# Optimization experiments

Measured on AMD Instinct MI355X. Metric: run time of the kernel, lower is better.

Reference implementation:

```python
import jax, jax.numpy as jnp
import numpy as np

B, S1, S2, S3, I, O = 4, 64, 64, 64, 32, 32
MX, MZ = 16, 16
HID = O * 2  # factor=2 feedforward hidden


def setup_inputs() -> dict:
    key = jax.random.key(0)
    ks = jax.random.split(key, 5)
    x = jax.random.normal(ks[0], (B, S1, S2, S3, I), jnp.float32)
    # xavier-normal-ish scale for complex fourier weights stored as [...,2]
    sw = np.float32(np.sqrt(2.0 / (I + O)))
    wx = jax.random.normal(ks[1], (I, O, MX, 2), jnp.float32) * sw
    wz = jax.random.normal(ks[2], (I, O, MZ, 2), jnp.float32) * sw
    w1 = jax.random.normal(ks[3], (O, HID), jnp.float32) * np.float32(np.sqrt(1.0 / O))
    b1 = jnp.zeros((HID,), jnp.float32)
    w2 = jax.random.normal(ks[4], (HID, O), jnp.float32) * np.float32(np.sqrt(1.0 / HID))
    b2 = jnp.zeros((O,), jnp.float32)
    return {"x": x, "wx": wx, "wz": wz, "w1": w1, "b1": b1, "w2": w2, "b2": b2}


def _forward_fourier(x, wx, wz):
    # x: [b, i, s1, s2, s3]
    # z-axis branch
    cwz = wz[..., 0] + 1j * wz[..., 1]          # [i, o, mz] complex
    xfz = jnp.fft.rfft(x, axis=-1, norm='ortho')  # [b,i,s1,s2,S3//2+1]
    pz = jnp.einsum('bixyz,ioz->boxyz', xfz[..., :MZ], cwz)
    pz = jnp.pad(pz, ((0, 0), (0, 0), (0, 0), (0, 0), (0, S3 // 2 + 1 - MZ)))
    xz = jnp.fft.irfft(pz, n=S3, axis=-1, norm='ortho')
    # x-axis branch (note: modes_y branch contributes 0 in the source, xy=0.0)
    cwx = wx[..., 0] + 1j * wx[..., 1]          # [i, o, mx]
    xfx = jnp.fft.rfft(x, axis=2, norm='ortho')  # [b,i,S1//2+1,s2,s3]
    px = jnp.einsum('bixyz,iox->boxyz', xfx[:, :, :MX], cwx)
    px = jnp.pad(px, ((0, 0), (0, 0), (0, S1 // 2 + 1 - MX), (0, 0), (0, 0)))
    xx = jnp.fft.irfft(px, n=S1, axis=2, norm='ortho')
    return xx + xz


def reference(x, wx, wz, w1, b1, w2, b2):
    xt = jnp.transpose(x, (0, 4, 1, 2, 3))      # b i s1 s2 s3
    y = _forward_fourier(xt, wx, wz)
    y = jnp.transpose(y, (0, 2, 3, 4, 1))       # b s1 s2 s3 o
    # backcast FeedForward: Linear -> ReLU -> Linear (dropout=0, no norms)
    h = jax.nn.relu(y @ w1 + b1)
    b_out = h @ w2 + b2
    return b_out
```

## Files before the change

### kernel.cpp

```cpp
#include <hip/hip_runtime.h>

namespace {

typedef _Float16 half_t;
typedef half_t f16x8 __attribute__((ext_vector_type(8)));
typedef float f32x4 __attribute__((ext_vector_type(4)));

constexpr size_t RSTR = 64 * 64 * 32;

constexpr int WS_TF = 0;
constexpr int WS_TI = 2048;
constexpr int WS_WZ = 4096;
constexpr int WS_WX = 69632;
constexpr int WS_W1 = 135168;
constexpr int WS_W2 = 137216;

__device__ __forceinline__ float f4get(const float4& v, int u) {
  return u == 0 ? v.x : (u == 1 ? v.y : (u == 2 ? v.z : v.w));
}

__device__ __forceinline__ f32x4 mfma16(f16x8 a, f16x8 b, f32x4 c) {
  return __builtin_amdgcn_mfma_f32_16x16x32_f16(a, b, c, 0, 0, 0);
}

__global__ __launch_bounds__(256) void kinit(const float* __restrict__ wx,
                                             const float* __restrict__ wz,
                                             const float* __restrict__ w1,
                                             const float* __restrict__ w2,
                                             half_t* __restrict__ wsh) {
  const int id = blockIdx.x * 256 + threadIdx.x;
  const int l = id & 63, r = l & 15, g = l >> 4;
  f16x8 frag;
  if (id < 256) {
    int fid = id >> 6, mt = fid >> 1, kt = fid & 1;
#pragma unroll
    for (int e = 0; e < 8; ++e) {
      int k = kt * 32 + 8 * g + e;
      int mc = mt * 16 + r, m = mc >> 1, p = mc & 1;
      float s, c;
      sincospif((float)(m * k) * (1.0f / 32.0f), &s, &c);
      frag[e] = (half_t)(0.125f * (p ? -s : c));
    }
    *(f16x8*)(wsh + WS_TF + (size_t)id * 8) = frag;
  } else if (id < 512) {
    int id2 = id - 256, mt = id2 >> 6;
#pragma unroll
    for (int e = 0; e < 8; ++e) {
      int zp = mt * 16 + r;
      int k = 8 * g + e, m = k >> 1, p = k & 1;
      float s, c;
      sincospif((float)(m * zp) * (1.0f / 32.0f), &s, &c);
      float sc = (m == 0) ? 0.125f : 0.25f;
      frag[e] = (half_t)(p ? -sc * s : sc * c);
    }
    *(f16x8*)(wsh + WS_TI + (size_t)id2 * 8) = frag;
  } else if (id < 16896) {
    int id2 = id - 512;
    const float* wsrc = wz;
    size_t off = WS_WZ;
    if (id2 >= 8192) { id2 -= 8192; wsrc = wx; off = WS_WX; }
    int fid = id2 >> 6, m = fid >> 3, kt = (fid >> 2) & 1, nt = fid & 3;
#pragma unroll
    for (int e = 0; e < 8; ++e) {
      int k = kt * 32 + 8 * g + e, i = k >> 1, p = k & 1;
      int n = nt * 16 + r, o = n >> 1, q = n & 1;
      int base = ((i * 32 + o) * 16 + m) * 2;
      float re = wsrc[base], im = wsrc[base + 1];
      frag[e] = (half_t)(q ? (p ? re : im) : (p ? -im : re));
    }
    *(f16x8*)(wsh + off + (size_t)id2 * 8) = frag;
  } else if (id < 17152) {
    int id2 = id - 16896, nt = id2 >> 6;
#pragma unroll
    for (int e = 0; e < 8; ++e) {
      int k = 8 * g + e, n = nt * 16 + r;
      frag[e] = (half_t)w1[k * 64 + n];
    }
    *(f16x8*)(wsh + WS_W1 + (size_t)id2 * 8) = frag;
  } else if (id < 17408) {
    int id2 = id - 17152, fid = id2 >> 6, kt = fid >> 1, nt = fid & 1;
#pragma unroll
    for (int e = 0; e < 8; ++e) {
      int k = kt * 32 + 8 * g + e, n = nt * 16 + r;
      frag[e] = (half_t)w2[k * 32 + n];
    }
    *(f16x8*)(wsh + WS_W2 + (size_t)id2 * 8) = frag;
  }
}

template <int BR>
__global__ __launch_bounds__(256) void kspec(const float* __restrict__ x,
                                             const half_t* __restrict__ wsh,
                                             const float* __restrict__ b1g,
                                             const float* __restrict__ b2g,
                                             float* __restrict__ outf) {
  __shared__ __align__(16) char smraw[49152];
  half_t* XB = (half_t*)smraw;
  half_t* FB = (half_t*)smraw;
  half_t* PB = (half_t*)(smraw + 32768);
  half_t* outh = (half_t*)outf;
  const int t = threadIdx.x, l = t & 63, w = t >> 6, r = l & 15, g = l >> 4;
  const f32x4 vzero = {0.f, 0.f, 0.f, 0.f};

  const int col0 = blockIdx.x * 8;
  size_t xbase = (size_t)col0 * 2048, zstr = 32, cstr = 2048;

  {
    int c = t >> 5, sub = t & 31;
    int i4 = (sub & 7) * 4, zq = sub >> 3;
    const float* xp = x + xbase + (size_t)c * cstr + i4;
#pragma unroll
    for (int zo = 0; zo < 2; ++zo) {
      int zb = zq * 16 + zo * 8;
      float4 v[8];
#pragma unroll
      for (int zz = 0; zz < 8; ++zz)
        v[zz] = *(const float4*)(xp + (size_t)(zb + zz) * zstr);
#pragma unroll
      for (int u = 0; u < 4; ++u) {
        f16x8 rowv;
#pragma unroll
        for (int zz = 0; zz < 8; ++zz) rowv[zz] = (half_t)f4get(v[zz], u);
        int rowi = c * 32 + i4 + u;
        int gr = (zb >> 3) ^ (rowi & 7);
        *(f16x8*)(XB + rowi * 64 + gr * 8) = rowv;
      }
    }
  }
  __syncthreads();

  f32x4 fa[2][4];
#pragma unroll
  for (int mt = 0; mt < 2; ++mt)
#pragma unroll
    for (int nt = 0; nt < 4; ++nt) fa[mt][nt] = vzero;
  {
    f16x8 Atf[2][2], Bx[4][2];
#pragma unroll
    for (int mt = 0; mt < 2; ++mt)
#pragma unroll
      for (int kt = 0; kt < 2; ++kt)
        Atf[mt][kt] = *(const f16x8*)(wsh + WS_TF + (size_t)((mt * 2 + kt) * 64 + l) * 8);
#pragma unroll
    for (int nt = 0; nt < 4; ++nt)
#pragma unroll
      for (int kt = 0; kt < 2; ++kt) {
        int rowi = w * 64 + nt * 16 + r;
        int gr = (kt * 4 + g) ^ (rowi & 7);
        Bx[nt][kt] = *(const f16x8*)(XB + rowi * 64 + gr * 8);
      }
#pragma unroll
    for (int kt = 0; kt < 2; ++kt)
#pragma unroll
      for (int nt = 0; nt < 4; ++nt)
#pragma unroll
        for (int mt = 0; mt < 2; ++mt)
          fa[mt][nt] = mfma16(Atf[mt][kt], Bx[nt][kt], fa[mt][nt]);
  }
  __syncthreads();

#pragma unroll
  for (int mt = 0; mt < 2; ++mt)
#pragma unroll
    for (int nt = 0; nt < 4; ++nt)
#pragma unroll
      for (int q = 0; q < 4; ++q) {
        int mc = mt * 16 + 4 * g + q, m = mc >> 1, p = mc & 1;
        int n = w * 64 + nt * 16 + r, c = n >> 5, i = n & 31;
        int k = 2 * i + p;
        FB[(m * 16 + c) * 64 + ((k >> 3) ^ (c & 7)) * 8 + (k & 7)] = (half_t)fa[mt][nt][q];
      }
  __syncthreads();

  const half_t* WF = wsh + WS_WZ;
#pragma unroll
  for (int j = 0; j < 4; ++j) {
    int m = w * 4 + j;
    f16x8 Af[2];
#pragma unroll
    for (int kt = 0; kt < 2; ++kt) {
      int gr = (kt * 4 + g) ^ (r & 7);
      Af[kt] = *(const f16x8*)(FB + (m * 16 + r) * 64 + gr * 8);
    }
    f32x4 pa[4];
#pragma unroll
    for (int nt = 0; nt < 4; ++nt) pa[nt] = vzero;
#pragma unroll
    for (int kt = 0; kt < 2; ++kt)
#pragma unroll
      for (int nt = 0; nt < 4; ++nt) {
        f16x8 Bw = *(const f16x8*)(WF + (size_t)((m * 8 + kt * 4 + nt) * 64 + l) * 8);
        pa[nt] = mfma16(Af[kt], Bw, pa[nt]);
      }
#pragma unroll
    for (int nt = 0; nt < 4; ++nt)
#pragma unroll
      for (int q = 0; q < 4; ++q) {
        int c = 4 * g + q;
        if (c < 8) {
          int n = nt * 16 + r, o = n >> 1, q2 = n & 1;
          int k = 2 * m + q2;
          PB[(c * 32 + o) * 32 + ((k >> 3) ^ (o & 3)) * 8 + (k & 7)] = (half_t)pa[nt][q];
        }
      }
  }
  __syncthreads();

  {
    f16x8 Ati[4];
#pragma unroll
    for (int mt = 0; mt < 4; ++mt)
      Ati[mt] = *(const f16x8*)(wsh + WS_TI + (size_t)(mt * 64 + l) * 8);
#pragma unroll
    for (int cc = 0; cc < 2; ++cc) {
      int c = w * 2 + cc;
      f16x8 Bp[2];
#pragma unroll
      for (int nt = 0; nt < 2; ++nt) {
        int o = nt * 16 + r;
        Bp[nt] = *(const f16x8*)(PB + (c * 32 + o) * 32 + (g ^ (o & 3)) * 8);
      }
      f32x4 ya[4][2];
#pragma unroll
      for (int mt = 0; mt < 4; ++mt)
#pragma unroll
        for (int nt = 0; nt < 2; ++nt) ya[mt][nt] = mfma16(Ati[mt], Bp[nt], vzero);
#pragma unroll
      for (int mt = 0; mt < 4; ++mt)
#pragma unroll
        for (int nt = 0; nt < 2; ++nt)
#pragma unroll
          for (int q = 0; q < 4; ++q) {
            int zp = mt * 16 + 4 * g + q, o = nt * 16 + r;
            outh[(size_t)(col0 + c) * 4096 + zp * 64 + o] = (half_t)ya[mt][nt][q];
          }
    }
  }
}

__global__ __launch_bounds__(256, 5) void kx4(const float* __restrict__ x,
                                              const half_t* __restrict__ wsh,
                                              const float* __restrict__ b1g,
                                              const float* __restrict__ b2g,
                                              float* __restrict__ outf) {
  __shared__ __align__(16) half_t smh[16384];
  half_t* XB = smh;
  half_t* FB = smh + 8192;
  half_t* PB = smh + 12288;
  half_t* YL = smh;
  half_t* HL = smh + 8192;
  half_t* outh = (half_t*)outf;
  const int t = threadIdx.x, l = t & 63, w = t >> 6, r = l & 15, g = l >> 4;
  const f32x4 vzero = {0.f, 0.f, 0.f, 0.f};

  const int d = blockIdx.x;
  const int p = (d & 7) * 512 + (d >> 3);
  const int col0 = p * 4;
  const int b = col0 >> 12, s2 = (col0 >> 6) & 63, s30 = col0 & 63;
  const size_t xbase = (size_t)b * 8388608 + (size_t)s2 * 2048 + (size_t)s30 * 32;

  {
    int sub = t & 31, zq = t >> 5;
    int c = sub >> 3, i4 = (sub & 7) * 4;
    const float* xp = x + xbase + (size_t)c * 32 + i4 + (size_t)(zq * 8) * RSTR;
    float4 v[8];
#pragma unroll
    for (int zz = 0; zz < 8; ++zz) v[zz] = *(const float4*)(xp + (size_t)zz * RSTR);
#pragma unroll
    for (int uu = 0; uu < 4; ++uu) {
      int u = (uu + sub) & 3;
      f16x8 rowv;
#pragma unroll
      for (int zz = 0; zz < 8; ++zz) rowv[zz] = (half_t)f4get(v[zz], u);
      int rowi = c * 32 + i4 + u;
      *(f16x8*)(XB + rowi * 64 + (zq ^ (rowi & 7)) * 8) = rowv;
    }
  }
  __syncthreads();

  f32x4 fa[2][2];
  {
    f16x8 Atf[2][2], Bx[2][2];
#pragma unroll
    for (int mt = 0; mt < 2; ++mt)
#pragma unroll
      for (int kt = 0; kt < 2; ++kt)
        Atf[mt][kt] = *(const f16x8*)(wsh + WS_TF + (size_t)((mt * 2 + kt) * 64 + l) * 8);
#pragma unroll
    for (int nt = 0; nt < 2; ++nt)
#pragma unroll
      for (int kt = 0; kt < 2; ++kt) {
        int rowi = w * 32 + nt * 16 + r;
        Bx[nt][kt] = *(const f16x8*)(XB + rowi * 64 + (((kt * 4 + g) ^ (rowi & 7))) * 8);
      }
#pragma unroll
    for (int mt = 0; mt < 2; ++mt)
#pragma unroll
      for (int nt = 0; nt < 2; ++nt) fa[mt][nt] = vzero;
#pragma unroll
    for (int kt = 0; kt < 2; ++kt)
#pragma unroll
      for (int nt = 0; nt < 2; ++nt)
#pragma unroll
        for (int mt = 0; mt < 2; ++mt)
          fa[mt][nt] = mfma16(Atf[mt][kt], Bx[nt][kt], fa[mt][nt]);
  }
#pragma unroll
  for (int mt = 0; mt < 2; ++mt)
#pragma unroll
    for (int nt = 0; nt < 2; ++nt)
#pragma unroll
      for (int q = 0; q < 4; ++q) {
        int mc = mt * 16 + 4 * g + q, m = mc >> 1, pp = mc & 1;
        int n = w * 32 + nt * 16 + r, c = n >> 5, i = n & 31;
        int k = 2 * i + pp;
        FB[(m * 4 + c) * 64 + (((k >> 3) ^ ((m + 2 * c) & 7))) * 8 + (k & 7)] =
            (half_t)fa[mt][nt][q];
      }
  __syncthreads();

#pragma unroll
  for (int j = 0; j < 4; ++j) {
    int m = w * 4 + j;
    int rsel = r & 3, keym = (m + 2 * rsel) & 7;
    f16x8 Af[2];
#pragma unroll
    for (int kt = 0; kt < 2; ++kt)
      Af[kt] = *(const f16x8*)(FB + (m * 4 + rsel) * 64 + (((kt * 4 + g) ^ keym)) * 8);
    f32x4 pa[4];
#pragma unroll
    for (int nt = 0; nt < 4; ++nt) pa[nt] = vzero;
#pragma unroll
    for (int kt = 0; kt < 2; ++kt)
#pragma unroll
      for (int nt = 0; nt < 4; ++nt) {
        f16x8 Bw = *(const f16x8*)(wsh + WS_WX + (size_t)((m * 8 + kt * 4 + nt) * 64 + l) * 8);
        pa[nt] = mfma16(Af[kt], Bw, pa[nt]);
      }
    if (g == 0) {
#pragma unroll
      for (int nt = 0; nt < 4; ++nt)
#pragma unroll
        for (int q = 0; q < 4; ++q) {
          int c = q;
          int n = nt * 16 + r, o = n >> 1, q2 = n & 1;
          int k = 2 * m + q2;
          PB[(c * 32 + o) * 32 + (((k >> 3) ^ (o & 3))) * 8 + (k & 7)] = (half_t)pa[nt][q];
        }
    }
  }
  __syncthreads();

  {
    half_t yzr[4][2][4];
    const half_t* yzp = outh + ((size_t)b * 4096 + s2) * 4096 + (size_t)(s30 + w) * 64 +
                        (size_t)(4 * g) * 262144 + r;
#pragma unroll
    for (int mt = 0; mt < 4; ++mt)
#pragma unroll
      for (int q = 0; q < 4; ++q)
#pragma unroll
        for (int nt = 0; nt < 2; ++nt)
          yzr[mt][nt][q] = yzp[(size_t)(mt * 16 + q) * 262144 + nt * 16];

    f16x8 Ati[4], Bp[2];
#pragma unroll
    for (int mt = 0; mt < 4; ++mt)
      Ati[mt] = *(const f16x8*)(wsh + WS_TI + (size_t)(mt * 64 + l) * 8);
#pragma unroll
    for (int nt = 0; nt < 2; ++nt) {
      int o = nt * 16 + r;
      Bp[nt] = *(const f16x8*)(PB + (w * 32 + o) * 32 + ((g ^ (o & 3))) * 8);
    }
    f32x4 ya[4][2];
#pragma unroll
    for (int mt = 0; mt < 4; ++mt)
#pragma unroll
      for (int nt = 0; nt < 2; ++nt) ya[mt][nt] = mfma16(Ati[mt], Bp[nt], vzero);
#pragma unroll
    for (int mt = 0; mt < 4; ++mt)
#pragma unroll
      for (int nt = 0; nt < 2; ++nt)
#pragma unroll
        for (int q = 0; q < 4; ++q) {
          int zp = mt * 16 + 4 * g + q, o = nt * 16 + r;
          float acc = ya[mt][nt][q] + (float)yzr[mt][nt][q];
          int rowi = w * 64 + zp;
          YL[rowi * 32 + (((o >> 3) ^ ((rowi >> 2) & 3))) * 8 + (o & 7)] = (half_t)acc;
        }
  }
  __syncthreads();

  {
    f16x8 W1F[4], W2F[4];
#pragma unroll
    for (int nt = 0; nt < 4; ++nt)
      W1F[nt] = *(const f16x8*)(wsh + WS_W1 + (size_t)(nt * 64 + l) * 8);
#pragma unroll
    for (int f = 0; f < 4; ++f)
      W2F[f] = *(const f16x8*)(wsh + WS_W2 + (size_t)(f * 64 + l) * 8);
    float b1v[4], b2v[2];
#pragma unroll
    for (int nt = 0; nt < 4; ++nt) b1v[nt] = b1g[nt * 16 + r];
#pragma unroll
    for (int nt = 0; nt < 2; ++nt) b2v[nt] = b2g[nt * 16 + r];

    for (int rr = 0; rr < 4; ++rr) {
      int rowA = rr * 64 + w * 16 + r;
      f16x8 AY = *(const f16x8*)(YL + rowA * 32 + ((g ^ ((rowA >> 2) & 3))) * 8);
      f32x4 ha[4];
#pragma unroll
      for (int nt = 0; nt < 4; ++nt) ha[nt] = mfma16(AY, W1F[nt], vzero);
#pragma unroll
      for (int nt = 0; nt < 4; ++nt)
#pragma unroll
        for (int q = 0; q < 4; ++q) {
          int rloc = w * 16 + 4 * g + q, n = nt * 16 + r;
          float hv = fmaxf(ha[nt][q] + b1v[nt], 0.f);
          HL[rloc * 64 + (((n >> 3) ^ ((rloc >> 2) & 7))) * 8 + (n & 7)] = (half_t)hv;
        }
      __syncthreads();
      int rowA2 = w * 16 + r;
      f16x8 AH[2];
#pragma unroll
      for (int kt = 0; kt < 2; ++kt)
        AH[kt] = *(const f16x8*)(HL + rowA2 * 64 + (((kt * 4 + g) ^ ((rowA2 >> 2) & 7))) * 8);
      f32x4 oa[2];
#pragma unroll
      for (int nt = 0; nt < 2; ++nt) oa[nt] = vzero;
#pragma unroll
      for (int kt = 0; kt < 2; ++kt)
#pragma unroll
        for (int nt = 0; nt < 2; ++nt) oa[nt] = mfma16(AH[kt], W2F[kt * 2 + nt], oa[nt]);
#pragma unroll
      for (int nt = 0; nt < 2; ++nt)
#pragma unroll
        for (int q = 0; q < 4; ++q) {
          int zp2 = w * 16 + 4 * g + q, o = nt * 16 + r;
          outf[(size_t)b * 8388608 + (size_t)zp2 * RSTR + (size_t)s2 * 2048 +
               (size_t)(s30 + rr) * 32 + o] = oa[nt][q] + b2v[nt];
        }
      if (rr < 3) __syncthreads();
    }
  }
}

}

extern "C" void kernel_launch(void* const* d_in, const int* in_sizes, int n_in,
                              void* d_out, int out_size, void* d_ws, size_t ws_size,
                              hipStream_t stream) {
  const float* x = (const float*)d_in[0];
  const float* wx = (const float*)d_in[1];
  const float* wz = (const float*)d_in[2];
  const float* w1 = (const float*)d_in[3];
  const float* b1 = (const float*)d_in[4];
  const float* w2 = (const float*)d_in[5];
  const float* b2 = (const float*)d_in[6];
  float* out = (float*)d_out;
  half_t* wsh = (half_t*)d_ws;

  hipLaunchKernelGGL(kinit, dim3(68), dim3(256), 0, stream, wx, wz, w1, w2, wsh);
  hipLaunchKernelGGL((kspec<0>), dim3(2048), dim3(256), 0, stream, x, wsh, b1, b2, out);
  hipLaunchKernelGGL(kx4, dim3(4096), dim3(256), 0, stream, x, wsh, b1, b2, out);
}
```

Measured before the change: 135.5 us.

## Hoist global loads early, pack FB stores, and halve FFN sync rounds

Issues the yz half-precision gather and the W1/W2/bias fragment loads at kernel start, before the LDS stages, so their latency overlaps the DFT and mode-mixing work. FB writes are packed as f16x2 pairs. The feed-forward loop now processes two 16-row tiles per wave per iteration, which cuts the number of block barriers from 7 to 3. Occupancy hint drops from 5 to 4 blocks per CU to make room for the extra live registers.

```diff
diff --git a/kernel.cpp b/kernel.cpp
--- a/kernel.cpp
+++ b/kernel.cpp
@@ -3,6 +3,7 @@
 namespace {
 
 typedef _Float16 half_t;
+typedef half_t f16x2 __attribute__((ext_vector_type(2)));
 typedef half_t f16x8 __attribute__((ext_vector_type(8)));
 typedef float f32x4 __attribute__((ext_vector_type(4)));
 
@@ -238,7 +239,7 @@
   }
 }
 
-__global__ __launch_bounds__(256, 5) void kx4(const float* __restrict__ x,
+__global__ __launch_bounds__(256, 4) void kx4(const float* __restrict__ x,
                                               const half_t* __restrict__ wsh,
                                               const float* __restrict__ b1g,
                                               const float* __restrict__ b2g,
@@ -259,20 +260,34 @@
   const int b = col0 >> 12, s2 = (col0 >> 6) & 63, s30 = col0 & 63;
   const size_t xbase = (size_t)b * 8388608 + (size_t)s2 * 2048 + (size_t)s30 * 32;
 
-  {
-    int sub = t & 31, zq = t >> 5;
-    int c = sub >> 3, i4 = (sub & 7) * 4;
-    const float* xp = x + xbase + (size_t)c * 32 + i4 + (size_t)(zq * 8) * RSTR;
-    float4 v[8];
-#pragma unroll
-    for (int zz = 0; zz < 8; ++zz) v[zz] = *(const float4*)(xp + (size_t)zz * RSTR);
+  const int sub = t & 31, zq = t >> 5;
+  const int sc = sub >> 3, si4 = (sub & 7) * 4;
+  const float* xp = x + xbase + (size_t)sc * 32 + si4 + (size_t)(zq * 8) * RSTR;
+  float4 v[8];
+#pragma unroll
+  for (int zz = 0; zz < 8; ++zz) v[zz] = *(const float4*)(xp + (size_t)zz * RSTR);
+
+  half_t yzr[4][2][4];
+  {
+    const half_t* yzp = outh + ((size_t)b * 4096 + s2) * 4096 + (size_t)(s30 + w) * 64 +
+                        (size_t)(4 * g) * 262144 + r;
+#pragma unroll
+    for (int mt = 0; mt < 4; ++mt)
+#pragma unroll
+      for (int q = 0; q < 4; ++q)
+#pragma unroll
+        for (int nt = 0; nt < 2; ++nt)
+          yzr[mt][nt][q] = yzp[(size_t)(mt * 16 + q) * 262144 + nt * 16];
+  }
+
+  {
 #pragma unroll
     for (int uu = 0; uu < 4; ++uu) {
       int u = (uu + sub) & 3;
       f16x8 rowv;
 #pragma unroll
       for (int zz = 0; zz < 8; ++zz) rowv[zz] = (half_t)f4get(v[zz], u);
-      int rowi = c * 32 + i4 + u;
+      int rowi = sc * 32 + si4 + u;
       *(f16x8*)(XB + rowi * 64 + (zq ^ (rowi & 7)) * 8) = rowv;
     }
   }
@@ -310,12 +325,14 @@
 #pragma unroll
     for (int nt = 0; nt < 2; ++nt)
 #pragma unroll
-      for (int q = 0; q < 4; ++q) {
-        int mc = mt * 16 + 4 * g + q, m = mc >> 1, pp = mc & 1;
+      for (int pr = 0; pr < 2; ++pr) {
+        int q = 2 * pr;
+        int mc = mt * 16 + 4 * g + q, m = mc >> 1;
         int n = w * 32 + nt * 16 + r, c = n >> 5, i = n & 31;
-        int k = 2 * i + pp;
-        FB[(m * 4 + c) * 64 + (((k >> 3) ^ ((m + 2 * c) & 7))) * 8 + (k & 7)] =
-            (half_t)fa[mt][nt][q];
+        int k = 2 * i;
+        f16x2 pairv = {(half_t)fa[mt][nt][q], (half_t)fa[mt][nt][q + 1]};
+        *(f16x2*)(FB + (m * 4 + c) * 64 + (((k >> 3) ^ ((m + 2 * c) & 7))) * 8 + (k & 7)) =
+            pairv;
       }
   __syncthreads();
 
@@ -349,20 +366,22 @@
         }
     }
   }
-  __syncthreads();
-
-  {
-    half_t yzr[4][2][4];
-    const half_t* yzp = outh + ((size_t)b * 4096 + s2) * 4096 + (size_t)(s30 + w) * 64 +
-                        (size_t)(4 * g) * 262144 + r;
-#pragma unroll
-    for (int mt = 0; mt < 4; ++mt)
-#pragma unroll
-      for (int q = 0; q < 4; ++q)
-#pragma unroll
-        for (int nt = 0; nt < 2; ++nt)
-          yzr[mt][nt][q] = yzp[(size_t)(mt * 16 + q) * 262144 + nt * 16];
-
+
+  f16x8 W1F[4], W2F[4];
+#pragma unroll
+  for (int nt = 0; nt < 4; ++nt)
+    W1F[nt] = *(const f16x8*)(wsh + WS_W1 + (size_t)(nt * 64 + l) * 8);
+#pragma unroll
+  for (int f = 0; f < 4; ++f)
+    W2F[f] = *(const f16x8*)(wsh + WS_W2 + (size_t)(f * 64 + l) * 8);
+  float b1v[4], b2v[2];
+#pragma unroll
+  for (int nt = 0; nt < 4; ++nt) b1v[nt] = b1g[nt * 16 + r];
+#pragma unroll
+  for (int nt = 0; nt < 2; ++nt) b2v[nt] = b2g[nt * 16 + r];
+  __syncthreads();
+
+  {
     f16x8 Ati[4], Bp[2];
 #pragma unroll
     for (int mt = 0; mt < 4; ++mt)
@@ -391,57 +410,61 @@
   }
   __syncthreads();
 
-  {
-    f16x8 W1F[4], W2F[4];
-#pragma unroll
-    for (int nt = 0; nt < 4; ++nt)
-      W1F[nt] = *(const f16x8*)(wsh + WS_W1 + (size_t)(nt * 64 + l) * 8);
-#pragma unroll
-    for (int f = 0; f < 4; ++f)
-      W2F[f] = *(const f16x8*)(wsh + WS_W2 + (size_t)(f * 64 + l) * 8);
-    float b1v[4], b2v[2];
-#pragma unroll
-    for (int nt = 0; nt < 4; ++nt) b1v[nt] = b1g[nt * 16 + r];
-#pragma unroll
-    for (int nt = 0; nt < 2; ++nt) b2v[nt] = b2g[nt * 16 + r];
-
-    for (int rr = 0; rr < 4; ++rr) {
-      int rowA = rr * 64 + w * 16 + r;
-      f16x8 AY = *(const f16x8*)(YL + rowA * 32 + ((g ^ ((rowA >> 2) & 3))) * 8);
-      f32x4 ha[4];
-#pragma unroll
-      for (int nt = 0; nt < 4; ++nt) ha[nt] = mfma16(AY, W1F[nt], vzero);
+  for (int rr = 0; rr < 2; ++rr) {
+    f16x8 AY[2];
+#pragma unroll
+    for (int mt = 0; mt < 2; ++mt) {
+      int rowA = rr * 128 + w * 32 + mt * 16 + r;
+      AY[mt] = *(const f16x8*)(YL + rowA * 32 + ((g ^ ((rowA >> 2) & 3))) * 8);
+    }
+    f32x4 ha[2][4];
+#pragma unroll
+    for (int mt = 0; mt < 2; ++mt)
+#pragma unroll
+      for (int nt = 0; nt < 4; ++nt) ha[mt][nt] = mfma16(AY[mt], W1F[nt], vzero);
+#pragma unroll
+    for (int mt = 0; mt < 2; ++mt)
 #pragma unroll
       for (int nt = 0; nt < 4; ++nt)
 #pragma unroll
         for (int q = 0; q < 4; ++q) {
-          int rloc = w * 16 + 4 * g + q, n = nt * 16 + r;
-          float hv = fmaxf(ha[nt][q] + b1v[nt], 0.f);
+          int rloc = w * 32 + mt * 16 + 4 * g + q, n = nt * 16 + r;
+          float hv = fmaxf(ha[mt][nt][q] + b1v[nt], 0.f);
           HL[rloc * 64 + (((n >> 3) ^ ((rloc >> 2) & 7))) * 8 + (n & 7)] = (half_t)hv;
         }
-      __syncthreads();
-      int rowA2 = w * 16 + r;
-      f16x8 AH[2];
-#pragma unroll
-      for (int kt = 0; kt < 2; ++kt)
-        AH[kt] = *(const f16x8*)(HL + rowA2 * 64 + (((kt * 4 + g) ^ ((rowA2 >> 2) & 7))) * 8);
-      f32x4 oa[2];
-#pragma unroll
-      for (int nt = 0; nt < 2; ++nt) oa[nt] = vzero;
-#pragma unroll
-      for (int kt = 0; kt < 2; ++kt)
-#pragma unroll
-        for (int nt = 0; nt < 2; ++nt) oa[nt] = mfma16(AH[kt], W2F[kt * 2 + nt], oa[nt]);
+    __syncthreads();
+    f16x8 AH[2][2];
+#pragma unroll
+    for (int mt = 0; mt < 2; ++mt)
+#pragma unroll
+      for (int kt = 0; kt < 2; ++kt) {
+        int rowA2 = w * 32 + mt * 16 + r;
+        AH[mt][kt] = *(const f16x8*)(HL + rowA2 * 64 + (((kt * 4 + g) ^ ((rowA2 >> 2) & 7))) * 8);
+      }
+    f32x4 oa[2][2];
+#pragma unroll
+    for (int mt = 0; mt < 2; ++mt)
+#pragma unroll
+      for (int nt = 0; nt < 2; ++nt) oa[mt][nt] = vzero;
+#pragma unroll
+    for (int kt = 0; kt < 2; ++kt)
+#pragma unroll
+      for (int mt = 0; mt < 2; ++mt)
+#pragma unroll
+        for (int nt = 0; nt < 2; ++nt)
+          oa[mt][nt] = mfma16(AH[mt][kt], W2F[kt * 2 + nt], oa[mt][nt]);
+#pragma unroll
+    for (int mt = 0; mt < 2; ++mt)
 #pragma unroll
       for (int nt = 0; nt < 2; ++nt)
 #pragma unroll
         for (int q = 0; q < 4; ++q) {
-          int zp2 = w * 16 + 4 * g + q, o = nt * 16 + r;
-          outf[(size_t)b * 8388608 + (size_t)zp2 * RSTR + (size_t)s2 * 2048 +
-               (size_t)(s30 + rr) * 32 + o] = oa[nt][q] + b2v[nt];
+          int rowg = rr * 128 + w * 32 + mt * 16 + 4 * g + q;
+          int c = rowg >> 6, zp = rowg & 63, o = nt * 16 + r;
+          outf[(size_t)b * 8388608 + (size_t)zp * RSTR + (size_t)s2 * 2048 +
+               (size_t)(s30 + c) * 32 + o] = oa[mt][nt][q] + b2v[nt];
         }
-      if (rr < 3) __syncthreads();
-    }
+    if (rr == 0) __syncthreads();
   }
 }
 
```

Result: slower. 145.8 us (+7.6%).

## Make feedforward stage wave-private to drop block barriers and vectorize yz loads

Applied to the files above, without the earlier changes.

Reorganizes the final stage of the kx4 kernel so each wave owns one s3 column's 64 z-rows in YL and uses private double-buffered H scratch in LDS. This removes the block-wide __syncthreads between the iFFT stage and the feedforward stage and inside its loop. The z-branch partial is now read as 8-wide f16 vectors and added in f16 before the first matmul, instead of scalar strided loads added in fp32. Also packs pairs of f16 stores into FB, changes the XB swizzle key, and lowers the launch-bounds occupancy hint from 5 to 4. Adding the z-branch in f16 loses some precision, and the lower occupancy hint lets the compiler use more registers.

```diff
diff --git a/kernel.cpp b/kernel.cpp
--- a/kernel.cpp
+++ b/kernel.cpp
@@ -3,6 +3,7 @@
 namespace {
 
 typedef _Float16 half_t;
+typedef half_t f16x2 __attribute__((ext_vector_type(2)));
 typedef half_t f16x8 __attribute__((ext_vector_type(8)));
 typedef float f32x4 __attribute__((ext_vector_type(4)));
 
@@ -238,7 +239,7 @@
   }
 }
 
-__global__ __launch_bounds__(256, 5) void kx4(const float* __restrict__ x,
+__global__ __launch_bounds__(256, 4) void kx4(const float* __restrict__ x,
                                               const half_t* __restrict__ wsh,
                                               const float* __restrict__ b1g,
                                               const float* __restrict__ b2g,
@@ -248,14 +249,15 @@
   half_t* FB = smh + 8192;
   half_t* PB = smh + 12288;
   half_t* YL = smh;
-  half_t* HL = smh + 8192;
+  half_t* HLa = smh + 8192;
+  half_t* HLb = smh + 12288;
   half_t* outh = (half_t*)outf;
   const int t = threadIdx.x, l = t & 63, w = t >> 6, r = l & 15, g = l >> 4;
   const f32x4 vzero = {0.f, 0.f, 0.f, 0.f};
 
   const int d = blockIdx.x;
-  const int p = (d & 7) * 512 + (d >> 3);
-  const int col0 = p * 4;
+  const int pp = (d & 7) * 512 + (d >> 3);
+  const int col0 = pp * 4;
   const int b = col0 >> 12, s2 = (col0 >> 6) & 63, s30 = col0 & 63;
   const size_t xbase = (size_t)b * 8388608 + (size_t)s2 * 2048 + (size_t)s30 * 32;
 
@@ -267,13 +269,13 @@
 #pragma unroll
     for (int zz = 0; zz < 8; ++zz) v[zz] = *(const float4*)(xp + (size_t)zz * RSTR);
 #pragma unroll
-    for (int uu = 0; uu < 4; ++uu) {
-      int u = (uu + sub) & 3;
+    for (int u = 0; u < 4; ++u) {
       f16x8 rowv;
 #pragma unroll
       for (int zz = 0; zz < 8; ++zz) rowv[zz] = (half_t)f4get(v[zz], u);
       int rowi = c * 32 + i4 + u;
-      *(f16x8*)(XB + rowi * 64 + (zq ^ (rowi & 7)) * 8) = rowv;
+      int key = (rowi ^ (rowi >> 2)) & 7;
+      *(f16x8*)(XB + rowi * 64 + (zq ^ key) * 8) = rowv;
     }
   }
   __syncthreads();
@@ -291,7 +293,8 @@
 #pragma unroll
       for (int kt = 0; kt < 2; ++kt) {
         int rowi = w * 32 + nt * 16 + r;
-        Bx[nt][kt] = *(const f16x8*)(XB + rowi * 64 + (((kt * 4 + g) ^ (rowi & 7))) * 8);
+        int key = (rowi ^ (rowi >> 2)) & 7;
+        Bx[nt][kt] = *(const f16x8*)(XB + rowi * 64 + (((kt * 4 + g) ^ key)) * 8);
       }
 #pragma unroll
     for (int mt = 0; mt < 2; ++mt)
@@ -310,12 +313,14 @@
 #pragma unroll
     for (int nt = 0; nt < 2; ++nt)
 #pragma unroll
-      for (int q = 0; q < 4; ++q) {
-        int mc = mt * 16 + 4 * g + q, m = mc >> 1, pp = mc & 1;
+      for (int pr = 0; pr < 2; ++pr) {
+        int q = 2 * pr;
+        int mc = mt * 16 + 4 * g + q, m = mc >> 1;
         int n = w * 32 + nt * 16 + r, c = n >> 5, i = n & 31;
-        int k = 2 * i + pp;
-        FB[(m * 4 + c) * 64 + (((k >> 3) ^ ((m + 2 * c) & 7))) * 8 + (k & 7)] =
-            (half_t)fa[mt][nt][q];
+        int k = 2 * i;
+        f16x2 pairv = {(half_t)fa[mt][nt][q], (half_t)fa[mt][nt][q + 1]};
+        *(f16x2*)(FB + (m * 4 + c) * 64 + (((k >> 3) ^ ((m + 2 * c) & 7))) * 8 + (k & 7)) =
+            pairv;
       }
   __syncthreads();
 
@@ -351,27 +356,33 @@
   }
   __syncthreads();
 
-  {
-    half_t yzr[4][2][4];
-    const half_t* yzp = outh + ((size_t)b * 4096 + s2) * 4096 + (size_t)(s30 + w) * 64 +
-                        (size_t)(4 * g) * 262144 + r;
-#pragma unroll
-    for (int mt = 0; mt < 4; ++mt)
-#pragma unroll
-      for (int q = 0; q < 4; ++q)
-#pragma unroll
-        for (int nt = 0; nt < 2; ++nt)
-          yzr[mt][nt][q] = yzp[(size_t)(mt * 16 + q) * 262144 + nt * 16];
-
-    f16x8 Ati[4], Bp[2];
-#pragma unroll
-    for (int mt = 0; mt < 4; ++mt)
-      Ati[mt] = *(const f16x8*)(wsh + WS_TI + (size_t)(mt * 64 + l) * 8);
-#pragma unroll
-    for (int nt = 0; nt < 2; ++nt) {
-      int o = nt * 16 + r;
-      Bp[nt] = *(const f16x8*)(PB + (w * 32 + o) * 32 + ((g ^ (o & 3))) * 8);
-    }
+  f16x8 Bp[2];
+#pragma unroll
+  for (int nt = 0; nt < 2; ++nt) {
+    int o = nt * 16 + r;
+    Bp[nt] = *(const f16x8*)(PB + (w * 32 + o) * 32 + ((g ^ (o & 3))) * 8);
+  }
+  f16x8 Ati[4];
+#pragma unroll
+  for (int mt = 0; mt < 4; ++mt)
+    Ati[mt] = *(const f16x8*)(wsh + WS_TI + (size_t)(mt * 64 + l) * 8);
+  f16x8 yzf[4];
+#pragma unroll
+  for (int rr = 0; rr < 4; ++rr) {
+    int zp = rr * 16 + r;
+    yzf[rr] = *(const f16x8*)(outh + ((size_t)(b * 64 + zp) * 64 + s2) * 4096 +
+                              (size_t)(s30 + w) * 64 + 8 * g);
+  }
+  f16x8 W1F[4];
+#pragma unroll
+  for (int nt = 0; nt < 4; ++nt)
+    W1F[nt] = *(const f16x8*)(wsh + WS_W1 + (size_t)(nt * 64 + l) * 8);
+  float b1v[4];
+#pragma unroll
+  for (int nt = 0; nt < 4; ++nt) b1v[nt] = b1g[nt * 16 + r];
+
+  half_t* YLw = YL + w * 2048;
+  {
     f32x4 ya[4][2];
 #pragma unroll
     for (int mt = 0; mt < 4; ++mt)
@@ -384,64 +395,55 @@
 #pragma unroll
         for (int q = 0; q < 4; ++q) {
           int zp = mt * 16 + 4 * g + q, o = nt * 16 + r;
-          float acc = ya[mt][nt][q] + (float)yzr[mt][nt][q];
-          int rowi = w * 64 + zp;
-          YL[rowi * 32 + (((o >> 3) ^ ((rowi >> 2) & 3))) * 8 + (o & 7)] = (half_t)acc;
+          YLw[zp * 32 + (((o >> 3) ^ ((zp >> 2) & 3))) * 8 + (o & 7)] = (half_t)ya[mt][nt][q];
         }
   }
-  __syncthreads();
-
-  {
-    f16x8 W1F[4], W2F[4];
+  f16x8 W2F[4];
+#pragma unroll
+  for (int f = 0; f < 4; ++f)
+    W2F[f] = *(const f16x8*)(wsh + WS_W2 + (size_t)(f * 64 + l) * 8);
+  float b2v[2];
+#pragma unroll
+  for (int nt = 0; nt < 2; ++nt) b2v[nt] = b2g[nt * 16 + r];
+
+  half_t* HLwa = HLa + w * 1024;
+  half_t* HLwb = HLb + w * 1024;
+#pragma unroll
+  for (int rr = 0; rr < 4; ++rr) {
+    half_t* HLw = (rr & 1) ? HLwb : HLwa;
+    int rowl = rr * 16 + r;
+    f16x8 AY = *(const f16x8*)(YLw + rowl * 32 + ((g ^ ((rowl >> 2) & 3))) * 8);
+    AY = AY + yzf[rr];
+    f32x4 ha[4];
+#pragma unroll
+    for (int nt = 0; nt < 4; ++nt) ha[nt] = mfma16(AY, W1F[nt], vzero);
 #pragma unroll
     for (int nt = 0; nt < 4; ++nt)
-      W1F[nt] = *(const f16x8*)(wsh + WS_W1 + (size_t)(nt * 64 + l) * 8);
-#pragma unroll
-    for (int f = 0; f < 4; ++f)
-      W2F[f] = *(const f16x8*)(wsh + WS_W2 + (size_t)(f * 64 + l) * 8);
-    float b1v[4], b2v[2];
-#pragma unroll
-    for (int nt = 0; nt < 4; ++nt) b1v[nt] = b1g[nt * 16 + r];
-#pragma unroll
-    for (int nt = 0; nt < 2; ++nt) b2v[nt] = b2g[nt * 16 + r];
-
-    for (int rr = 0; rr < 4; ++rr) {
-      int rowA = rr * 64 + w * 16 + r;
-      f16x8 AY = *(const f16x8*)(YL + rowA * 32 + ((g ^ ((rowA >> 2) & 3))) * 8);
-      f32x4 ha[4];
-#pragma unroll
-      for (int nt = 0; nt < 4; ++nt) ha[nt] = mfma16(AY, W1F[nt], vzero);
-#pragma unroll
-      for (int nt = 0; nt < 4; ++nt)
-#pragma unroll
-        for (int q = 0; q < 4; ++q) {
-          int rloc = w * 16 + 4 * g + q, n = nt * 16 + r;
-          float hv = fmaxf(ha[nt][q] + b1v[nt], 0.f);
-          HL[rloc * 64 + (((n >> 3) ^ ((rloc >> 2) & 7))) * 8 + (n & 7)] = (half_t)hv;
-        }
-      __syncthreads();
-      int rowA2 = w * 16 + r;
-      f16x8 AH[2];
-#pragma unroll
-      for (int kt = 0; kt < 2; ++kt)
-        AH[kt] = *(const f16x8*)(HL + rowA2 * 64 + (((kt * 4 + g) ^ ((rowA2 >> 2) & 7))) * 8);
-      f32x4 oa[2];
-#pragma unroll
-      for (int nt = 0; nt < 2; ++nt) oa[nt] = vzero;
-#pragma unroll
-      for (int kt = 0; kt < 2; ++kt)
-#pragma unroll
-        for (int nt = 0; nt < 2; ++nt) oa[nt] = mfma16(AH[kt], W2F[kt * 2 + nt], oa[nt]);
-#pragma unroll
-      for (int nt = 0; nt < 2; ++nt)
-#pragma unroll
-        for (int q = 0; q < 4; ++q) {
-          int zp2 = w * 16 + 4 * g + q, o = nt * 16 + r;
-          outf[(size_t)b * 8388608 + (size_t)zp2 * RSTR + (size_t)s2 * 2048 +
-               (size_t)(s30 + rr) * 32 + o] = oa[nt][q] + b2v[nt];
-        }
-      if (rr < 3) __syncthreads();
-    }
+#pragma unroll
+      for (int q = 0; q < 4; ++q) {
+        int row4 = 4 * g + q, n = nt * 16 + r;
+        float hv = fmaxf(ha[nt][q] + b1v[nt], 0.f);
+        HLw[row4 * 64 + (((n >> 3) ^ g)) * 8 + (n & 7)] = (half_t)hv;
+      }
+    f16x8 AH[2];
+#pragma unroll
+    for (int kt = 0; kt < 2; ++kt)
+      AH[kt] = *(const f16x8*)(HLw + r * 64 + (((kt * 4 + g) ^ (r >> 2))) * 8);
+    f32x4 oa[2];
+#pragma unroll
+    for (int nt = 0; nt < 2; ++nt) oa[nt] = vzero;
+#pragma unroll
+    for (int kt = 0; kt < 2; ++kt)
+#pragma unroll
+      for (int nt = 0; nt < 2; ++nt) oa[nt] = mfma16(AH[kt], W2F[kt * 2 + nt], oa[nt]);
+#pragma unroll
+    for (int nt = 0; nt < 2; ++nt)
+#pragma unroll
+      for (int q = 0; q < 4; ++q) {
+        int zp = rr * 16 + 4 * g + q, o = nt * 16 + r;
+        outf[(size_t)b * 8388608 + (size_t)zp * RSTR + (size_t)s2 * 2048 +
+             (size_t)(s30 + w) * 32 + o] = oa[nt][q] + b2v[nt];
+      }
   }
 }
 
```

New measurement: 134.8 us. About the same (-0.5%).
